# Performance work log

Measured on AMD Instinct MI355X. Metric: run time of the kernel, lower is better.

## Reference

```python
import jax, jax.numpy as jnp
import numpy as np

B, N, C, H = 8, 2048, 384, 6
D = C // H  # head dim = 64
SCALE = D ** -0.5


def setup_inputs() -> dict:
    key = jax.random.key(0)
    k1, k2, k3, k4 = jax.random.split(key, 4)
    x = jax.random.normal(k1, (B, N, C), dtype=jnp.float32)
    prompt = jnp.zeros((1,), dtype=jnp.float32)  # unused by forward
    mask = jax.random.uniform(k2, (B, N, N), dtype=jnp.float32)
    qkv_w = jax.random.normal(k3, (3 * C, C), dtype=jnp.float32) * (C ** -0.5)
    proj_w = jax.random.normal(k4, (C, C), dtype=jnp.float32) * (C ** -0.5)
    proj_b = jnp.zeros((C,), dtype=jnp.float32)
    return {"x": x, "prompt": prompt, "mask": mask,
            "qkv_w": qkv_w, "proj_w": proj_w, "proj_b": proj_b}


def reference(x, prompt, mask, qkv_w, proj_w, proj_b):
    b, n, c = x.shape
    # qkv: Linear(dim, 3*dim, bias=False) -> (B,N,3,H,D) -> (3,B,H,N,D)
    qkv = (x @ qkv_w.T).reshape(b, n, 3, H, D).transpose(2, 0, 3, 1, 4)
    q, k, v = qkv[0], qkv[1], qkv[2]
    # attn scores with additive mask (mask * -1e5), softmax over keys
    attn = jnp.einsum('bhqd,bhkd->bhqk', q, k) * SCALE
    attn = attn + (mask * -100000.0)[:, None, :, :]
    attn = jax.nn.softmax(attn, axis=-1)
    out = jnp.einsum('bhqk,bhkd->bhqd', attn, v)  # (B,H,N,D)
    out = out.transpose(0, 2, 1, 3).reshape(b, n, c)
    return out @ proj_w.T + proj_b
```

## Files before the change

### kernel.cpp

```cpp
#include <hip/hip_runtime.h>
#include <stdint.h>
#include <math.h>

#define BB 8
#define SEQ 2048
#define CDIM 384
#define NH 6
#define HD 64
#define QKVN 1152

typedef __attribute__((ext_vector_type(8))) __bf16 bf16x8;
typedef __attribute__((ext_vector_type(4))) float f32x4;
typedef __attribute__((ext_vector_type(4))) unsigned short ushort4v;

__device__ __forceinline__ unsigned short f2bf(float f) {
  unsigned int u = __float_as_uint(f);
  u += 0x7fffu + ((u >> 16) & 1u);
  return (unsigned short)(u >> 16);
}

__global__ void k_convert(const float* __restrict__ src, unsigned short* __restrict__ dst, int n4) {
  int i = blockIdx.x * blockDim.x + threadIdx.x;
  if (i >= n4) return;
  float4 f = reinterpret_cast<const float4*>(src)[i];
  ushort4v u;
  u.x = f2bf(f.x); u.y = f2bf(f.y); u.z = f2bf(f.z); u.w = f2bf(f.w);
  reinterpret_cast<ushort4v*>(dst)[i] = u;
}

__device__ __forceinline__ void gload_lds16(const unsigned short* g, unsigned short* l) {
  __builtin_amdgcn_global_load_lds((const __attribute__((address_space(1))) void*)g,
                                   (__attribute__((address_space(3))) void*)l, 16, 0, 0);
}

template<int OUT_F32>
__global__ __launch_bounds__(256, 2) void k_gemm_bt(
    const unsigned short* __restrict__ A, const unsigned short* __restrict__ Bm,
    unsigned short* __restrict__ Cb, float* __restrict__ Cf,
    const float* __restrict__ bias, int M, int Nc, int K)
{
  __shared__ unsigned short lA[128 * 32];
  __shared__ unsigned short lB[128 * 32];
  const int t = threadIdx.x;
  const int w = t >> 6, l = t & 63;
  const int wr = w >> 1, wc = w & 1;
  const int row0 = blockIdx.x * 128, col0 = blockIdx.y * 128;
  const f32x4 vzero = {0.f, 0.f, 0.f, 0.f};
  f32x4 acc[4][4];
#pragma unroll
  for (int m = 0; m < 4; ++m)
#pragma unroll
    for (int n = 0; n < 4; ++n) acc[m][n] = vzero;

  const int srow = w * 16 + (l >> 2);
  const int scol = (l & 3) * 8;
  const int lr = l & 15, kc = (l >> 4) * 8;

  for (int k0 = 0; k0 < K; k0 += 32) {
#pragma unroll
    for (int r = 0; r < 2; ++r) {
      gload_lds16(A + (size_t)(row0 + r * 64 + srow) * K + k0 + scol,
                  &lA[(r * 64 + srow) * 32 + scol]);
      gload_lds16(Bm + (size_t)(col0 + r * 64 + srow) * K + k0 + scol,
                  &lB[(r * 64 + srow) * 32 + scol]);
    }
    __syncthreads();
    bf16x8 af[4], bfr[4];
#pragma unroll
    for (int m = 0; m < 4; ++m)
      af[m] = *(const bf16x8*)&lA[(wr * 64 + m * 16 + lr) * 32 + kc];
#pragma unroll
    for (int n = 0; n < 4; ++n)
      bfr[n] = *(const bf16x8*)&lB[(wc * 64 + n * 16 + lr) * 32 + kc];
#pragma unroll
    for (int m = 0; m < 4; ++m)
#pragma unroll
      for (int n = 0; n < 4; ++n)
        acc[m][n] = __builtin_amdgcn_mfma_f32_16x16x32_bf16(af[m], bfr[n], acc[m][n], 0, 0, 0);
    __syncthreads();
  }

#pragma unroll
  for (int m = 0; m < 4; ++m) {
    const int row = row0 + wr * 64 + m * 16 + (l >> 4) * 4;
#pragma unroll
    for (int n = 0; n < 4; ++n) {
      const int col = col0 + wc * 64 + n * 16 + (l & 15);
      if (OUT_F32) {
        const float bv = bias[col];
#pragma unroll
        for (int j = 0; j < 4; ++j)
          Cf[(size_t)(row + j) * Nc + col] = acc[m][n][j] + bv;
      } else {
#pragma unroll
        for (int j = 0; j < 4; ++j)
          Cb[(size_t)(row + j) * Nc + col] = f2bf(acc[m][n][j]);
      }
    }
  }
}

__global__ void k_vtrans(const unsigned short* __restrict__ qkv, unsigned short* __restrict__ vt)
{
  __shared__ unsigned short tile[64][76];
  const int bh = blockIdx.x;
  const int b = bh / NH, h = bh - b * NH;
  const int n0 = blockIdx.y * 64;
  const int t = threadIdx.x;
  const int rr0 = t >> 4;
  const int c4 = (t & 15) * 4;
  const unsigned short* src = qkv + (size_t)(b * SEQ + n0) * QKVN + 2 * CDIM + h * HD;
#pragma unroll
  for (int rr = 0; rr < 4; ++rr) {
    int n = rr * 16 + rr0;
    ushort4v v = *(const ushort4v*)(src + (size_t)n * QKVN + c4);
    *(ushort4v*)&tile[n][c4] = v;
  }
  __syncthreads();
  unsigned short* dst = vt + (size_t)bh * HD * SEQ + n0;
#pragma unroll
  for (int rr = 0; rr < 4; ++rr) {
    int d = rr * 16 + rr0;
    ushort4v v;
    v.x = tile[c4 + 0][d];
    v.y = tile[c4 + 1][d];
    v.z = tile[c4 + 2][d];
    v.w = tile[c4 + 3][d];
    *(ushort4v*)(dst + (size_t)d * SEQ + c4) = v;
  }
}

__global__ __launch_bounds__(256, 4) void k_attn(
    const unsigned short* __restrict__ qkv, const float* __restrict__ mask,
    const unsigned short* __restrict__ vt, unsigned short* __restrict__ aout)
{
  const int bid = blockIdx.x;
  const int b = bid & 7;
  const int g2 = bid >> 3;
  const int h = g2 % NH;
  const int nt = g2 / NH;
  const int t = threadIdx.x;
  const int w = t >> 6, l = t & 63;
  const int gk = l >> 4, c = l & 15;
  const int q0 = nt * 64 + w * 16;

  __shared__ unsigned short lK[2][4096];
  __shared__ unsigned short lV[2][4096];
  __shared__ unsigned int lP[4][512];
  unsigned int* prow = lP[w] + c * 32;

  const unsigned short* qb = qkv + (size_t)(b * SEQ + q0) * QKVN + h * HD;
  const unsigned short* kb = qkv + (size_t)(b * SEQ) * QKVN + CDIM + h * HD;
  const unsigned short* vb = vt + (size_t)(b * NH + h) * HD * SEQ;
  const float* mrowc = mask + ((size_t)b * SEQ + q0 + c) * SEQ;

  const int trow = t >> 3, tg = t & 7;
  const int glog = tg ^ (trow & 7);
  const size_t kSrc = (size_t)trow * QKVN + glog * 8;
  const size_t vSrc = (size_t)trow * SEQ + glog * 8;

  const int fr0 = c * 64 + ((gk) ^ (c & 7)) * 8;
  const int fr1 = c * 64 + ((4 + gk) ^ (c & 7)) * 8;
  const int cx = (c & 7) << 2;

  bf16x8 qf0 = *(const bf16x8*)(qb + (size_t)c * QKVN + gk * 8);
  bf16x8 qf1 = *(const bf16x8*)(qb + (size_t)c * QKVN + 32 + gk * 8);
#pragma unroll
  for (int i = 0; i < 8; ++i) {
    qf0[i] = (__bf16)((float)qf0[i] * 0.18033688f);
    qf1[i] = (__bf16)((float)qf1[i] * 0.18033688f);
  }

  const f32x4 vzero = {0.f, 0.f, 0.f, 0.f};
  f32x4 acco[4];
  float mreg = -INFINITY, asum = 0.f;
#pragma unroll
  for (int dt = 0; dt < 4; ++dt) acco[dt] = vzero;

#pragma unroll
  for (int j = 0; j < 2; ++j) {
    gload_lds16(kb + (size_t)j * 32 * QKVN + kSrc, &lK[0][j * 2048 + t * 8]);
    gload_lds16(vb + (size_t)j * 32 * SEQ + vSrc, &lV[0][j * 2048 + t * 8]);
  }
  float4 mk[4];
#pragma unroll
  for (int j = 0; j < 4; ++j)
    mk[j] = *(const float4*)(mrowc + 16 * j + 4 * gk);
  int buf = 0;

  for (int kt = 0; kt < SEQ; kt += 64) {
    const bool haveNext = (kt + 64 < SEQ);
    __syncthreads();
    if (haveNext) {
#pragma unroll
      for (int j = 0; j < 2; ++j) {
        gload_lds16(kb + (size_t)(kt + 64 + j * 32) * QKVN + kSrc, &lK[buf ^ 1][j * 2048 + t * 8]);
        gload_lds16(vb + (kt + 64) + (size_t)j * 32 * SEQ + vSrc, &lV[buf ^ 1][j * 2048 + t * 8]);
      }
    }

    f32x4 s[4];
#pragma unroll
    for (int j = 0; j < 4; ++j) {
      bf16x8 kfa = *(const bf16x8*)&lK[buf][j * 1024 + fr0];
      bf16x8 kfb = *(const bf16x8*)&lK[buf][j * 1024 + fr1];
      s[j] = __builtin_amdgcn_mfma_f32_16x16x32_bf16(kfa, qf0, vzero, 0, 0, 0);
      s[j] = __builtin_amdgcn_mfma_f32_16x16x32_bf16(kfb, qf1, s[j], 0, 0, 0);
    }

#pragma unroll
    for (int j = 0; j < 4; ++j) {
      const float* mkf = (const float*)&mk[j];
#pragma unroll
      for (int r = 0; r < 4; ++r)
        s[j][r] = fmaf(mkf[r], -144269.50f, s[j][r]);
    }

    if (haveNext) {
#pragma unroll
      for (int j = 0; j < 4; ++j)
        mk[j] = *(const float4*)(mrowc + kt + 64 + 16 * j + 4 * gk);
    }

    float tm = fmaxf(fmaxf(fmaxf(s[0][0], s[0][1]), fmaxf(s[0][2], s[0][3])),
                     fmaxf(fmaxf(s[1][0], s[1][1]), fmaxf(s[1][2], s[1][3])));
    tm = fmaxf(tm, fmaxf(fmaxf(fmaxf(s[2][0], s[2][1]), fmaxf(s[2][2], s[2][3])),
                         fmaxf(fmaxf(s[3][0], s[3][1]), fmaxf(s[3][2], s[3][3]))));
    tm = fmaxf(tm, __shfl_xor(tm, 16));
    tm = fmaxf(tm, __shfl_xor(tm, 32));

    if (__any(tm > mreg + 8.f)) {
      const float mn = fmaxf(mreg, tm);
      const float al = __builtin_amdgcn_exp2f(mreg - mn);
      mreg = mn;
      asum *= al;
      float alr[4];
#pragma unroll
      for (int r = 0; r < 4; ++r)
        alr[r] = __shfl(al, 20 * gk + r);
#pragma unroll
      for (int dt = 0; dt < 4; ++dt)
#pragma unroll
        for (int r = 0; r < 4; ++r)
          acco[dt][r] *= alr[r];
    }

#pragma unroll
    for (int j = 0; j < 4; ++j)
#pragma unroll
      for (int r = 0; r < 4; ++r)
        s[j][r] = __builtin_amdgcn_exp2f(s[j][r] - mreg);
    float rs = ((s[0][0] + s[0][1]) + (s[0][2] + s[0][3]))
             + ((s[1][0] + s[1][1]) + (s[1][2] + s[1][3]))
             + ((s[2][0] + s[2][1]) + (s[2][2] + s[2][3]))
             + ((s[3][0] + s[3][1]) + (s[3][2] + s[3][3]));
    rs += __shfl_xor(rs, 16);
    rs += __shfl_xor(rs, 32);
    asum += rs;

    unsigned int pk[8];
#pragma unroll
    for (int j = 0; j < 4; ++j) {
      asm("v_cvt_pk_bf16_f32 %0, %1, %2" : "=v"(pk[2 * j]) : "v"(s[j][0]), "v"(s[j][1]));
      asm("v_cvt_pk_bf16_f32 %0, %1, %2" : "=v"(pk[2 * j + 1]) : "v"(s[j][2]), "v"(s[j][3]));
    }
    __asm__ volatile("" ::: "memory");
#pragma unroll
    for (int j = 0; j < 4; ++j) {
      prow[(8 * j + 2 * gk + 0) ^ cx] = pk[2 * j];
      prow[(8 * j + 2 * gk + 1) ^ cx] = pk[2 * j + 1];
    }
    __asm__ volatile("" ::: "memory");
    bf16x8 pf0 = *(const bf16x8*)(prow + ((4 * gk) ^ cx));
    bf16x8 pf1 = *(const bf16x8*)(prow + ((16 + 4 * gk) ^ cx));
    __asm__ volatile("" ::: "memory");

#pragma unroll
    for (int dt = 0; dt < 4; ++dt) {
      bf16x8 vf0 = *(const bf16x8*)&lV[buf][dt * 1024 + fr0];
      bf16x8 vf1 = *(const bf16x8*)&lV[buf][dt * 1024 + fr1];
      acco[dt] = __builtin_amdgcn_mfma_f32_16x16x32_bf16(pf0, vf0, acco[dt], 0, 0, 0);
      acco[dt] = __builtin_amdgcn_mfma_f32_16x16x32_bf16(pf1, vf1, acco[dt], 0, 0, 0);
    }
    buf ^= 1;
  }

  float invr[4];
#pragma unroll
  for (int r = 0; r < 4; ++r)
    invr[r] = 1.0f / __shfl(asum, 20 * gk + r);
  unsigned short* ob = aout + (size_t)(b * SEQ + q0) * CDIM + h * HD;
#pragma unroll
  for (int r = 0; r < 4; ++r)
#pragma unroll
    for (int dt = 0; dt < 4; ++dt)
      ob[(size_t)(4 * gk + r) * CDIM + dt * 16 + c] = f2bf(acco[dt][r] * invr[r]);
}

extern "C" void kernel_launch(void* const* d_in, const int* in_sizes, int n_in,
                              void* d_out, int out_size, void* d_ws, size_t ws_size,
                              hipStream_t stream) {
  (void)in_sizes; (void)n_in; (void)out_size; (void)ws_size;
  const float* x      = (const float*)d_in[0];
  const float* mask   = (const float*)d_in[2];
  const float* qkv_w  = (const float*)d_in[3];
  const float* proj_w = (const float*)d_in[4];
  const float* proj_b = (const float*)d_in[5];
  float* out = (float*)d_out;
  char* ws = (char*)d_ws;

  unsigned short* xb    = (unsigned short*)(ws + 0);
  unsigned short* wqb   = (unsigned short*)(ws + 12582912);
  unsigned short* wpb   = (unsigned short*)(ws + 13467648);
  unsigned short* qkvb  = (unsigned short*)(ws + 13762560);
  unsigned short* vtb   = (unsigned short*)(ws + 51511296);
  unsigned short* aoutb = (unsigned short*)(ws + 64094208);

  k_convert<<<6144, 256, 0, stream>>>(x, xb, 1572864);
  k_convert<<<432, 256, 0, stream>>>(qkv_w, wqb, 110592);
  k_convert<<<144, 256, 0, stream>>>(proj_w, wpb, 36864);
  k_gemm_bt<0><<<dim3(128, 9), 256, 0, stream>>>(xb, wqb, qkvb, nullptr, nullptr, 16384, 1152, 384);
  k_vtrans<<<dim3(48, 32), 256, 0, stream>>>(qkvb, vtb);
  k_attn<<<1536, 256, 0, stream>>>(qkvb, mask, vtb, aoutb);
  k_gemm_bt<1><<<dim3(128, 3), 256, 0, stream>>>(aoutb, wpb, nullptr, out, proj_b, 16384, 384, 384);
}
```

Measured before the change: 191.1 us.

## Feed softmax probabilities to PV MFMA from registers, permuting V reads instead

The P matrix no longer makes a round trip through shared memory (pack, store, reload) before the PV matmul. The QK^T output fragment is used directly as the A operand, and the V fragment is gathered with four 8-byte LDS reads in a matching permuted k-order. This removes per-iteration LDS writes, reads and the associated waits and LDS usage. The cost is narrower V reads and a correctness dependency on the register layout matching.

```diff
diff --git a/kernel.cpp b/kernel.cpp
--- a/kernel.cpp
+++ b/kernel.cpp
@@ -10,6 +10,7 @@
 #define QKVN 1152
 
 typedef __attribute__((ext_vector_type(8))) __bf16 bf16x8;
+typedef __attribute__((ext_vector_type(4))) __bf16 bf16x4;
 typedef __attribute__((ext_vector_type(4))) float f32x4;
 typedef __attribute__((ext_vector_type(4))) unsigned short ushort4v;
 
@@ -146,22 +147,25 @@
 
   __shared__ unsigned short lK[2][4096];
   __shared__ unsigned short lV[2][4096];
-  __shared__ unsigned int lP[4][512];
-  unsigned int* prow = lP[w] + c * 32;
 
   const unsigned short* qb = qkv + (size_t)(b * SEQ + q0) * QKVN + h * HD;
   const unsigned short* kb = qkv + (size_t)(b * SEQ) * QKVN + CDIM + h * HD;
   const unsigned short* vb = vt + (size_t)(b * NH + h) * HD * SEQ;
-  const float* mrowc = mask + ((size_t)b * SEQ + q0 + c) * SEQ;
+  const float* mrowc = mask + ((size_t)b * SEQ + q0 + c) * SEQ + 4 * gk;
 
   const int trow = t >> 3, tg = t & 7;
   const int glog = tg ^ (trow & 7);
   const size_t kSrc = (size_t)trow * QKVN + glog * 8;
   const size_t vSrc = (size_t)trow * SEQ + glog * 8;
+  const int tid8 = t * 8;
 
   const int fr0 = c * 64 + ((gk) ^ (c & 7)) * 8;
   const int fr1 = c * 64 + ((4 + gk) ^ (c & 7)) * 8;
-  const int cx = (c & 7) << 2;
+  const int cx2 = 2 * (c & 7);
+  const int vg0 = c * 64 + ((gk) ^ cx2) * 4;
+  const int vg1 = c * 64 + ((4 + gk) ^ cx2) * 4;
+  const int vg2 = c * 64 + ((8 + gk) ^ cx2) * 4;
+  const int vg3 = c * 64 + ((12 + gk) ^ cx2) * 4;
 
   bf16x8 qf0 = *(const bf16x8*)(qb + (size_t)c * QKVN + gk * 8);
   bf16x8 qf1 = *(const bf16x8*)(qb + (size_t)c * QKVN + 32 + gk * 8);
@@ -179,13 +183,13 @@
 
 #pragma unroll
   for (int j = 0; j < 2; ++j) {
-    gload_lds16(kb + (size_t)j * 32 * QKVN + kSrc, &lK[0][j * 2048 + t * 8]);
-    gload_lds16(vb + (size_t)j * 32 * SEQ + vSrc, &lV[0][j * 2048 + t * 8]);
+    gload_lds16(kb + (size_t)j * 32 * QKVN + kSrc, &lK[0][j * 2048 + tid8]);
+    gload_lds16(vb + (size_t)j * 32 * SEQ + vSrc, &lV[0][j * 2048 + tid8]);
   }
   float4 mk[4];
 #pragma unroll
   for (int j = 0; j < 4; ++j)
-    mk[j] = *(const float4*)(mrowc + 16 * j + 4 * gk);
+    mk[j] = *(const float4*)(mrowc + 16 * j);
   int buf = 0;
 
   for (int kt = 0; kt < SEQ; kt += 64) {
@@ -194,8 +198,8 @@
     if (haveNext) {
 #pragma unroll
       for (int j = 0; j < 2; ++j) {
-        gload_lds16(kb + (size_t)(kt + 64 + j * 32) * QKVN + kSrc, &lK[buf ^ 1][j * 2048 + t * 8]);
-        gload_lds16(vb + (kt + 64) + (size_t)j * 32 * SEQ + vSrc, &lV[buf ^ 1][j * 2048 + t * 8]);
+        gload_lds16(kb + (size_t)(kt + 64 + j * 32) * QKVN + kSrc, &lK[buf ^ 1][j * 2048 + tid8]);
+        gload_lds16(vb + (kt + 64) + (size_t)j * 32 * SEQ + vSrc, &lV[buf ^ 1][j * 2048 + tid8]);
       }
     }
 
@@ -215,11 +219,10 @@
       for (int r = 0; r < 4; ++r)
         s[j][r] = fmaf(mkf[r], -144269.50f, s[j][r]);
     }
-
     if (haveNext) {
 #pragma unroll
       for (int j = 0; j < 4; ++j)
-        mk[j] = *(const float4*)(mrowc + kt + 64 + 16 * j + 4 * gk);
+        mk[j] = *(const float4*)(mrowc + kt + 64 + 16 * j);
     }
 
     float tm = fmaxf(fmaxf(fmaxf(s[0][0], s[0][1]), fmaxf(s[0][2], s[0][3])),
@@ -258,27 +261,24 @@
     rs += __shfl_xor(rs, 32);
     asum += rs;
 
-    unsigned int pk[8];
+    union { unsigned int u[8]; bf16x8 v[2]; } pu;
 #pragma unroll
     for (int j = 0; j < 4; ++j) {
-      asm("v_cvt_pk_bf16_f32 %0, %1, %2" : "=v"(pk[2 * j]) : "v"(s[j][0]), "v"(s[j][1]));
-      asm("v_cvt_pk_bf16_f32 %0, %1, %2" : "=v"(pk[2 * j + 1]) : "v"(s[j][2]), "v"(s[j][3]));
-    }
-    __asm__ volatile("" ::: "memory");
-#pragma unroll
-    for (int j = 0; j < 4; ++j) {
-      prow[(8 * j + 2 * gk + 0) ^ cx] = pk[2 * j];
-      prow[(8 * j + 2 * gk + 1) ^ cx] = pk[2 * j + 1];
-    }
-    __asm__ volatile("" ::: "memory");
-    bf16x8 pf0 = *(const bf16x8*)(prow + ((4 * gk) ^ cx));
-    bf16x8 pf1 = *(const bf16x8*)(prow + ((16 + 4 * gk) ^ cx));
-    __asm__ volatile("" ::: "memory");
+      asm("v_cvt_pk_bf16_f32 %0, %1, %2" : "=v"(pu.u[2 * j]) : "v"(s[j][0]), "v"(s[j][1]));
+      asm("v_cvt_pk_bf16_f32 %0, %1, %2" : "=v"(pu.u[2 * j + 1]) : "v"(s[j][2]), "v"(s[j][3]));
+    }
+    bf16x8 pf0 = pu.v[0];
+    bf16x8 pf1 = pu.v[1];
 
 #pragma unroll
     for (int dt = 0; dt < 4; ++dt) {
-      bf16x8 vf0 = *(const bf16x8*)&lV[buf][dt * 1024 + fr0];
-      bf16x8 vf1 = *(const bf16x8*)&lV[buf][dt * 1024 + fr1];
+      const unsigned short* vrow = &lV[buf][dt * 1024];
+      bf16x4 a0 = *(const bf16x4*)(vrow + vg0);
+      bf16x4 a1 = *(const bf16x4*)(vrow + vg1);
+      bf16x4 a2 = *(const bf16x4*)(vrow + vg2);
+      bf16x4 a3 = *(const bf16x4*)(vrow + vg3);
+      bf16x8 vf0 = __builtin_shufflevector(a0, a1, 0, 1, 2, 3, 4, 5, 6, 7);
+      bf16x8 vf1 = __builtin_shufflevector(a2, a3, 0, 1, 2, 3, 4, 5, 6, 7);
       acco[dt] = __builtin_amdgcn_mfma_f32_16x16x32_bf16(pf0, vf0, acco[dt], 0, 0, 0);
       acco[dt] = __builtin_amdgcn_mfma_f32_16x16x32_bf16(pf1, vf1, acco[dt], 0, 0, 0);
     }
```

Result: slower. 198.2 us (+3.7%).
